# Optimization experiments

Hardware: AMD Instinct MI355X
Metric: run time of the kernel (lower is better)

Reference implementation:

```python
import jax, jax.numpy as jnp
import numpy as np

HEADS = 8

def setup_inputs() -> dict:
    key = jax.random.key(0)
    ks = jax.random.split(key, 4)
    N, C, H, W = 8, 256, 128, 128
    s = 0.02  # conv weight init scale
    return {
        "x":  jax.random.normal(ks[0], (N, C, H, W), dtype=jnp.float32),
        "Wk": jax.random.normal(ks[1], (C, C), dtype=jnp.float32) * s,
        "bk": jnp.zeros((C,), dtype=jnp.float32),
        "Wq": jax.random.normal(ks[2], (C, C), dtype=jnp.float32) * s,
        "bq": jnp.zeros((C,), dtype=jnp.float32),
        "Wv": jax.random.normal(ks[3], (C, C), dtype=jnp.float32) * s,
        "bv": jnp.zeros((C,), dtype=jnp.float32),
    }

def _conv1x1(x, Wt, b):
    # 1x1 conv == per-pixel GEMM: [N,C,H,W] x [D,C] -> [N,D,H,W]
    return jnp.einsum('nchw,dc->ndhw', x, Wt) + b[None, :, None, None]

def reference(x, Wk, bk, Wq, bq, Wv, bv):
    N, C, H, W = x.shape
    hc = C // HEADS          # head_channels
    L = H * W                # spatial tokens
    k = _conv1x1(x, Wk, bk).reshape(N, HEADS, hc, L)
    q = _conv1x1(x, Wq, bq).reshape(N, HEADS, hc, L)
    v = _conv1x1(x, Wv, bv).reshape(N, HEADS, hc, L)
    k = jax.nn.softmax(k, axis=3)   # softmax over spatial dim (keys)
    q = jax.nn.softmax(q, axis=2)   # softmax over channel dim within head (queries)
    # context = key @ value^T : [N,HEADS,hc_k,hc_v]
    ctx = jnp.einsum('nhkl,nhvl->nhkv', k, v)
    # attended = context^T @ query : [N,HEADS,hc_v,L]
    att = jnp.einsum('nhkv,nhkl->nhvl', ctx, q)
    att = att.reshape(N, C, H, W)
    # dim == out_channels -> reprojection is None; residual add
    return att + x
```

## Files before the change

kernel.cpp:

```cpp
#include <hip/hip_runtime.h>


typedef __attribute__((ext_vector_type(8))) short short8;
typedef __attribute__((ext_vector_type(4))) float f32x4;
typedef long long ll;

#define NB     8
#define CCH    256
#define LSP    16384
#define NHEADS 8
#define HC     32
#define NT     32
#define WSC    0.015625f

__device__ __forceinline__ unsigned short f2bf(float f) {
  union { float f; unsigned u; } v; v.f = f;
  unsigned r = v.u + 0x7fffu + ((v.u >> 16) & 1u);
  return (unsigned short)(r >> 16);
}
__device__ __forceinline__ unsigned cvt_pk_bf16(float lo, float hi) {
  unsigned r;
  asm("v_cvt_pk_bf16_f32 %0, %1, %2" : "=v"(r) : "v"(lo), "v"(hi));
  return r;
}
__device__ __forceinline__ unsigned char f2fp8(float f) {
  union { float f; unsigned u; } v; v.f = f;
  unsigned s = (v.u >> 24) & 0x80u;
  unsigned x = v.u & 0x7FFFFFFFu;
  if (x < 0x3C800000u) {
    float a = fabsf(f);
    int q = (int)rintf(a * 512.f);
    return (unsigned char)(s | (unsigned)q);
  }
  unsigned r = x + 0xFFFFFu + ((x >> 20) & 1u);
  unsigned e = r >> 23;
  unsigned m = (r >> 20) & 7u;
  int fe = (int)e - 120;
  if (fe > 15 || (fe == 15 && m == 7)) return (unsigned char)(s | 0x7Eu);
  return (unsigned char)(s | ((unsigned)fe << 3) | m);
}
__device__ __forceinline__ void gload_lds16(const unsigned char* g, unsigned char* l) {
  __builtin_amdgcn_global_load_lds(
      (const __attribute__((address_space(1))) unsigned int*)g,
      (__attribute__((address_space(3))) unsigned int*)l, 16, 0, 0);
}

__global__ void k_prep(const float* __restrict__ Wk, const float* __restrict__ bk,
                       const float* __restrict__ Wq, const float* __restrict__ bq,
                       const float* __restrict__ Wv, const float* __restrict__ bv,
                       unsigned char* __restrict__ Wb, float* __restrict__ bb,
                       float* __restrict__ ctx, float* __restrict__ S) {
  int idx = blockIdx.x * 256 + threadIdx.x;
  if (idx < NHEADS * 96 * CCH) {
    int c = idx & (CCH - 1);
    int row = (idx >> 8) % 96;
    int h = idx / (96 * CCH);
    int ch = h * HC;
    float val;
    if (row < HC)          val = Wk[(ch + row) * CCH + c];
    else if (row < 2 * HC) val = Wv[(ch + row - HC) * CCH + c];
    else                   val = Wq[(ch + row - 2 * HC) * CCH + c];
    Wb[idx] = f2fp8(val * 64.f);
  }
  if (idx < NHEADS * 96) {
    int row = idx % 96, h = idx / 96, ch = h * HC;
    float val;
    if (row < HC)          val = bk[ch + row];
    else if (row < 2 * HC) val = bv[ch + row - HC];
    else                   val = bq[ch + row - 2 * HC];
    bb[idx] = val;
  }
  if (idx < NB * NHEADS * HC * HC) ctx[idx] = 0.f;
  if (idx < NB * NHEADS * HC)      S[idx]   = 0.f;
}

__global__ __launch_bounds__(256)
void k_transpose(const float* __restrict__ x, unsigned char* __restrict__ xT) {
  __shared__ float tile[64][65];
  int b = blockIdx.x;
  int ct = b & 3;
  int lt = (b >> 2) & 255;
  int n  = b >> 10;
  int c0 = ct * 64, l0 = lt * 64;
  int t = threadIdx.x;
  int li = t & 63, cr = t >> 6;
  const float* xp = x + (size_t)n * CCH * LSP;
#pragma unroll
  for (int i = 0; i < 16; ++i) {
    int ci = cr * 16 + i;
    tile[ci][li] = xp[(size_t)(c0 + ci) * LSP + l0 + li];
  }
  __syncthreads();
  int cq = t & 15, lg = t >> 4;
  unsigned char* xo = xT + ((size_t)n * LSP + l0) * CCH + c0;
#pragma unroll
  for (int i = 0; i < 4; ++i) {
    int l = lg * 4 + i;
    unsigned pk = 0;
#pragma unroll
    for (int j = 0; j < 4; ++j)
      pk |= ((unsigned)f2fp8(tile[cq * 4 + j][l])) << (8 * j);
    *(unsigned*)&xo[(size_t)l * CCH + cq * 4] = pk;
  }
}

__global__ __launch_bounds__(512)
void k_fused(const unsigned char* __restrict__ xT,
             const unsigned char* __restrict__ Wb, const float* __restrict__ bb,
             unsigned short* __restrict__ qbuf, float* __restrict__ ctx,
             float* __restrict__ S) {
  __shared__ unsigned char wlds[96 * 256];
  __shared__ unsigned char xt[2][128 * 256];
  __shared__ unsigned short ekst[2][32][136];
  __shared__ unsigned short vst[2][32][136];

  int bid = (int)blockIdx.x;
  int h = bid >> 5;
  int r5 = bid & 31;
  int n = r5 >> 2, q2 = r5 & 3;
  int l0 = q2 << 12;
  int nh = n * NHEADS + h;
  int tid = threadIdx.x;
  int wid = tid >> 6, lane = tid & 63;
  int r16 = lane & 15, kg = lane >> 4;
  int rh = wid >> 2;
  int pq = wid & 3;

  const unsigned char* xTn = xT + ((size_t)n << 14) * CCH;
  const unsigned char* Wh = Wb + (size_t)h * 96 * CCH;

  auto stage_xt = [&](int buf, int tt) {
    int lb = l0 + tt * 128;
#pragma unroll
    for (int i = 0; i < 4; ++i) {
      int p = wid * 4 + i;
      int px = p * 4 + (lane >> 4);
      int c16 = lane & 15;
      gload_lds16(xTn + ((size_t)(lb + px) << 8) + ((c16 ^ (px & 7)) << 4),
                  &xt[buf][p * 1024]);
    }
  };

#pragma unroll
  for (int i = 0; i < 3; ++i) {
    int p = wid * 3 + i;
    int row = p * 4 + (lane >> 4);
    int c16 = lane & 15;
    gload_lds16(Wh + ((size_t)row << 8) + ((c16 ^ (row & 7)) << 4), &wlds[p * 1024]);
  }
  stage_xt(0, 0);
  stage_xt(1, 1);

  float bw[3];
#pragma unroll
  for (int m = 0; m < 3; ++m) bw[m] = bb[h * 96 + rh * 48 + m * 16 + r16];
  float bq[2][4];
#pragma unroll
  for (int m = 0; m < 2; ++m)
#pragma unroll
    for (int r = 0; r < 4; ++r) bq[m][r] = bb[h * 96 + 64 + m * 16 + kg * 4 + r];

  f32x4 actx = {0.f, 0.f, 0.f, 0.f};
  float sk0 = 0.f, sk1 = 0.f;

  asm volatile("s_waitcnt vmcnt(4)" ::: "memory");
  __builtin_amdgcn_sched_barrier(0);
  __builtin_amdgcn_s_barrier();
  __builtin_amdgcn_sched_barrier(0);

  const int base_w = (rh * 48 + r16) * 256;
  const int base_x = (pq * 32 + r16) * 256;
  int kh = pq >> 1, cvf = pq & 1;

  for (int t = 0; t < NT; ++t) {
    int cur = t & 1, sb = t & 1, pb = sb ^ 1;
    if (t) {
#pragma unroll
      for (int ks = 0; ks < 2; ++ks) {
        int col = kh * 64 + ks * 32 + kg * 8;
        short8 a = *(const short8*)&ekst[pb][rh * 16 + r16][col];
        short8 b = *(const short8*)&vst[pb][cvf * 16 + r16][col];
        actx = __builtin_amdgcn_mfma_f32_16x16x32_bf16(a, b, actx, 0, 0, 0);
      }
    }
    f32x4 acc[3][2];
#pragma unroll
    for (int m = 0; m < 3; ++m) { acc[m][0] = (f32x4){0,0,0,0}; acc[m][1] = (f32x4){0,0,0,0}; }
    const unsigned char* xb = &xt[cur][0];
#pragma unroll
    for (int kk = 0; kk < 8; ++kk) {
      int sw = (((kk * 2 + (kg >> 1)) ^ (r16 & 7)) << 4) + ((kg & 1) << 3);
      ll wf0 = *(const ll*)&wlds[base_w + sw];
      ll wf1 = *(const ll*)&wlds[base_w + 4096 + sw];
      ll wf2 = *(const ll*)&wlds[base_w + 8192 + sw];
      ll xf0 = *(const ll*)&xb[base_x + sw];
      ll xf1 = *(const ll*)&xb[base_x + 4096 + sw];
      if (rh == 0) {
        acc[0][0] = __builtin_amdgcn_mfma_f32_16x16x32_fp8_fp8(xf0, wf0, acc[0][0], 0, 0, 0);
        acc[0][1] = __builtin_amdgcn_mfma_f32_16x16x32_fp8_fp8(xf1, wf0, acc[0][1], 0, 0, 0);
        acc[1][0] = __builtin_amdgcn_mfma_f32_16x16x32_fp8_fp8(xf0, wf1, acc[1][0], 0, 0, 0);
        acc[1][1] = __builtin_amdgcn_mfma_f32_16x16x32_fp8_fp8(xf1, wf1, acc[1][1], 0, 0, 0);
        acc[2][0] = __builtin_amdgcn_mfma_f32_16x16x32_fp8_fp8(xf0, wf2, acc[2][0], 0, 0, 0);
        acc[2][1] = __builtin_amdgcn_mfma_f32_16x16x32_fp8_fp8(xf1, wf2, acc[2][1], 0, 0, 0);
      } else {
        acc[0][0] = __builtin_amdgcn_mfma_f32_16x16x32_fp8_fp8(xf0, wf0, acc[0][0], 0, 0, 0);
        acc[0][1] = __builtin_amdgcn_mfma_f32_16x16x32_fp8_fp8(xf1, wf0, acc[0][1], 0, 0, 0);
        acc[1][0] = __builtin_amdgcn_mfma_f32_16x16x32_fp8_fp8(wf1, xf0, acc[1][0], 0, 0, 0);
        acc[1][1] = __builtin_amdgcn_mfma_f32_16x16x32_fp8_fp8(wf1, xf1, acc[1][1], 0, 0, 0);
        acc[2][0] = __builtin_amdgcn_mfma_f32_16x16x32_fp8_fp8(wf2, xf0, acc[2][0], 0, 0, 0);
        acc[2][1] = __builtin_amdgcn_mfma_f32_16x16x32_fp8_fp8(wf2, xf1, acc[2][1], 0, 0, 0);
      }
    }
    __builtin_amdgcn_s_barrier();
    if (t + 2 < NT) stage_xt(cur, t + 2);

    if (rh == 0) {
#pragma unroll
      for (int nf = 0; nf < 2; ++nf) {
        int col = pq * 32 + nf * 16 + kg * 4;
#pragma unroll
        for (int m = 0; m < 2; ++m) {
          float e0 = __expf(acc[m][nf][0] * WSC + bw[m]);
          float e1 = __expf(acc[m][nf][1] * WSC + bw[m]);
          float e2 = __expf(acc[m][nf][2] * WSC + bw[m]);
          float e3 = __expf(acc[m][nf][3] * WSC + bw[m]);
          if (m == 0) sk0 += e0 + e1 + e2 + e3; else sk1 += e0 + e1 + e2 + e3;
          uint2 u = {cvt_pk_bf16(e0, e1), cvt_pk_bf16(e2, e3)};
          *(uint2*)&ekst[sb][m * 16 + r16][col] = u;
        }
        {
          float v0 = acc[2][nf][0] * WSC + bw[2], v1 = acc[2][nf][1] * WSC + bw[2];
          float v2 = acc[2][nf][2] * WSC + bw[2], v3 = acc[2][nf][3] * WSC + bw[2];
          uint2 u = {cvt_pk_bf16(v0, v1), cvt_pk_bf16(v2, v3)};
          *(uint2*)&vst[sb][r16][col] = u;
        }
      }
    } else {
#pragma unroll
      for (int nf = 0; nf < 2; ++nf) {
        int col = pq * 32 + nf * 16 + kg * 4;
        {
          float v0 = acc[0][nf][0] * WSC + bw[0], v1 = acc[0][nf][1] * WSC + bw[0];
          float v2 = acc[0][nf][2] * WSC + bw[0], v3 = acc[0][nf][3] * WSC + bw[0];
          uint2 u = {cvt_pk_bf16(v0, v1), cvt_pk_bf16(v2, v3)};
          *(uint2*)&vst[sb][16 + r16][col] = u;
        }
        float ea[4], eb[4];
        float s = 0.f;
#pragma unroll
        for (int r = 0; r < 4; ++r) {
          ea[r] = __expf(acc[1][nf][r] * WSC + bq[0][r]);
          eb[r] = __expf(acc[2][nf][r] * WSC + bq[1][r]);
          s += ea[r] + eb[r];
        }
        s += __shfl_xor(s, 16);
        s += __shfl_xor(s, 32);
        float inv = 1.f / s;
        int l = l0 + t * 128 + pq * 32 + nf * 16 + r16;
        unsigned short* qb = qbuf + (((size_t)nh * LSP + l) << 5);
        uint2 u0 = {cvt_pk_bf16(ea[0] * inv, ea[1] * inv), cvt_pk_bf16(ea[2] * inv, ea[3] * inv)};
        uint2 u1 = {cvt_pk_bf16(eb[0] * inv, eb[1] * inv), cvt_pk_bf16(eb[2] * inv, eb[3] * inv)};
        *(uint2*)&qb[kg * 4]      = u0;
        *(uint2*)&qb[16 + kg * 4] = u1;
      }
    }
    asm volatile("s_waitcnt lgkmcnt(0)" ::: "memory");
    __builtin_amdgcn_sched_barrier(0);
    if (t < NT - 2) {
      if (rh == 0) { asm volatile("s_waitcnt vmcnt(4)" ::: "memory"); }
      else         { asm volatile("s_waitcnt vmcnt(12)" ::: "memory"); }
    } else if (t == NT - 2) {
      if (rh == 0) { asm volatile("s_waitcnt vmcnt(0)" ::: "memory"); }
      else         { asm volatile("s_waitcnt vmcnt(8)" ::: "memory"); }
    }
    __builtin_amdgcn_sched_barrier(0);
    __builtin_amdgcn_s_barrier();
    __builtin_amdgcn_sched_barrier(0);
  }

#pragma unroll
  for (int ks = 0; ks < 2; ++ks) {
    int col = kh * 64 + ks * 32 + kg * 8;
    short8 a = *(const short8*)&ekst[(NT - 1) & 1][rh * 16 + r16][col];
    short8 b = *(const short8*)&vst[(NT - 1) & 1][cvf * 16 + r16][col];
    actx = __builtin_amdgcn_mfma_f32_16x16x32_bf16(a, b, actx, 0, 0, 0);
  }
  float* cp = ctx + ((size_t)nh << 10);
#pragma unroll
  for (int r = 0; r < 4; ++r)
    atomicAdd(&cp[(rh * 16 + kg * 4 + r) * HC + cvf * 16 + r16], actx[r]);
  if (rh == 0) {
    float s0 = sk0, s1 = sk1;
    s0 += __shfl_xor(s0, 16); s0 += __shfl_xor(s0, 32);
    s1 += __shfl_xor(s1, 16); s1 += __shfl_xor(s1, 32);
    if (kg == 0) {
      atomicAdd(&S[nh * HC + r16], s0);
      atomicAdd(&S[nh * HC + 16 + r16], s1);
    }
  }
}

__global__ void k_norm(const float* __restrict__ ctx, const float* __restrict__ S,
                       unsigned short* __restrict__ ctxT) {
  int idx = blockIdx.x * 256 + threadIdx.x;
  int cv = idx & 31, ck = (idx >> 5) & 31, nh = idx >> 10;
  float v = ctx[idx] / S[(nh << 5) + ck];
  ctxT[(nh << 10) + (cv << 5) + ck] = f2bf(v);
}

__global__ __launch_bounds__(256)
void k_att(const float* __restrict__ x, const unsigned short* __restrict__ qbuf,
           const unsigned short* __restrict__ ctxT, float* __restrict__ out) {
  int b = blockIdx.x;
  int lc = b & 63;
  int nh = b >> 6;
  int h = nh & 7, n = nh >> 3;
  int tid = threadIdx.x, wid = tid >> 6, lane = tid & 63;
  int r16 = lane & 15, kg = lane >> 4;
  int lw = lc * 256 + wid * 64;

  const unsigned short* cp = ctxT + ((size_t)nh << 10);
  short8 a0 = *(const short8*)&cp[(r16 << 5) + kg * 8];
  short8 a1 = *(const short8*)&cp[((16 + r16) << 5) + kg * 8];
  const unsigned short* qb = qbuf + (((size_t)nh * LSP) << 5);
  const float* xp = x   + ((size_t)n * CCH + (size_t)h * HC) * LSP;
  float*       op = out + ((size_t)n * CCH + (size_t)h * HC) * LSP;

#pragma unroll
  for (int t = 0; t < 4; ++t) {
    int l = lw + t * 16;
    short8 bf = *(const short8*)&qb[((size_t)(l + r16) << 5) + kg * 8];
    f32x4 d0 = {0, 0, 0, 0}, d1 = {0, 0, 0, 0};
    d0 = __builtin_amdgcn_mfma_f32_16x16x32_bf16(a0, bf, d0, 0, 0, 0);
    d1 = __builtin_amdgcn_mfma_f32_16x16x32_bf16(a1, bf, d1, 0, 0, 0);
#pragma unroll
    for (int r = 0; r < 4; ++r) {
      int cv = kg * 4 + r;
      int li = l + r16;
      op[(size_t)cv * LSP + li]        = d0[r] + xp[(size_t)cv * LSP + li];
      op[(size_t)(cv + 16) * LSP + li] = d1[r] + xp[(size_t)(cv + 16) * LSP + li];
    }
  }
}

extern "C" void kernel_launch(void* const* d_in, const int* in_sizes, int n_in,
                              void* d_out, int out_size, void* d_ws, size_t ws_size,
                              hipStream_t stream) {
  (void)in_sizes; (void)n_in; (void)out_size; (void)ws_size;
  const float* x  = (const float*)d_in[0];
  const float* Wk = (const float*)d_in[1];
  const float* bk = (const float*)d_in[2];
  const float* Wq = (const float*)d_in[3];
  const float* bq = (const float*)d_in[4];
  const float* Wv = (const float*)d_in[5];
  const float* bv = (const float*)d_in[6];
  float* out = (float*)d_out;

  char* ws = (char*)d_ws;
  unsigned char*  Wb   = (unsigned char*)(ws + 0);
  float*          bbp  = (float*)(ws + 196608);
  float*          ctx  = (float*)(ws + 199680);
  unsigned short* ctxT = (unsigned short*)(ws + 461824);
  float*          S    = (float*)(ws + 592896);
  unsigned short* qbuf = (unsigned short*)(ws + 601088);
  unsigned char*  xT   = (unsigned char*)(ws + 67709952);

  k_prep<<<768, 256, 0, stream>>>(Wk, bk, Wq, bq, Wv, bv, Wb, bbp, ctx, S);
  k_transpose<<<NB * 256 * 4, 256, 0, stream>>>(x, xT);
  k_fused<<<256, 512, 0, stream>>>(xT, Wb, bbp, qbuf, ctx, S);
  k_norm<<<256, 256, 0, stream>>>(ctx, S, ctxT);
  k_att<<<NB * NHEADS * 64, 256, 0, stream>>>(x, qbuf, ctxT, out);
}
```

Baseline: 193.9 us.

## Store queries and context in fp8, use hardware fp8 converts, rework LDS swizzles

The softmaxed query buffer and normalized context are now stored as fp8 instead of bf16, so the attention kernel runs fp8 MFMAs and reads half as many bytes of q. The transpose and q paths use the v_cvt_pk_fp8_f32 hardware instruction in place of software rounding. The LDS layouts for the e^k and v strips switch to a padded XOR swizzle, the x and W tile swizzles widen from 8 to 16 chunks, setprio is raised around the MFMA loop, and the vmcnt waits are changed to match the smaller store count. In exchange, fp8 for q and ctx loses precision, and hardware saturation and rounding may differ from the old software conversion.

```diff
diff --git a/kernel.cpp b/kernel.cpp
--- a/kernel.cpp
+++ b/kernel.cpp
@@ -21,6 +21,13 @@
 __device__ __forceinline__ unsigned cvt_pk_bf16(float lo, float hi) {
   unsigned r;
   asm("v_cvt_pk_bf16_f32 %0, %1, %2" : "=v"(r) : "v"(lo), "v"(hi));
+  return r;
+}
+__device__ __forceinline__ unsigned cvt4_fp8(float a, float b, float c, float d) {
+  unsigned r;
+  asm("v_cvt_pk_fp8_f32 %0, %1, %2\n\t"
+      "v_cvt_pk_fp8_f32 %0, %3, %4 op_sel:[0,0,1]"
+      : "=v"(r) : "v"(a), "v"(b), "v"(c), "v"(d));
   return r;
 }
 __device__ __forceinline__ unsigned char f2fp8(float f) {
@@ -43,6 +50,11 @@
   __builtin_amdgcn_global_load_lds(
       (const __attribute__((address_space(1))) unsigned int*)g,
       (__attribute__((address_space(3))) unsigned int*)l, 16, 0, 0);
+}
+__device__ __forceinline__ int strip_off(int row, int colsh) {
+  int byte = colsh * 2;
+  int chunk = byte >> 4;
+  return row * 272 + (((chunk ^ (row & 7)) << 4) | (byte & 15));
 }
 
 __global__ void k_prep(const float* __restrict__ Wk, const float* __restrict__ bk,
@@ -96,10 +108,8 @@
 #pragma unroll
   for (int i = 0; i < 4; ++i) {
     int l = lg * 4 + i;
-    unsigned pk = 0;
-#pragma unroll
-    for (int j = 0; j < 4; ++j)
-      pk |= ((unsigned)f2fp8(tile[cq * 4 + j][l])) << (8 * j);
+    unsigned pk = cvt4_fp8(tile[cq * 4][l], tile[cq * 4 + 1][l],
+                           tile[cq * 4 + 2][l], tile[cq * 4 + 3][l]);
     *(unsigned*)&xo[(size_t)l * CCH + cq * 4] = pk;
   }
 }
@@ -107,12 +117,12 @@
 __global__ __launch_bounds__(512)
 void k_fused(const unsigned char* __restrict__ xT,
              const unsigned char* __restrict__ Wb, const float* __restrict__ bb,
-             unsigned short* __restrict__ qbuf, float* __restrict__ ctx,
+             unsigned char* __restrict__ qbuf, float* __restrict__ ctx,
              float* __restrict__ S) {
   __shared__ unsigned char wlds[96 * 256];
   __shared__ unsigned char xt[2][128 * 256];
-  __shared__ unsigned short ekst[2][32][136];
-  __shared__ unsigned short vst[2][32][136];
+  __shared__ __align__(16) unsigned char ekst[2][32 * 272];
+  __shared__ __align__(16) unsigned char vst[2][32 * 272];
 
   int bid = (int)blockIdx.x;
   int h = bid >> 5;
@@ -136,7 +146,7 @@
       int p = wid * 4 + i;
       int px = p * 4 + (lane >> 4);
       int c16 = lane & 15;
-      gload_lds16(xTn + ((size_t)(lb + px) << 8) + ((c16 ^ (px & 7)) << 4),
+      gload_lds16(xTn + ((size_t)(lb + px) << 8) + ((c16 ^ (px & 15)) << 4),
                   &xt[buf][p * 1024]);
     }
   };
@@ -146,7 +156,7 @@
     int p = wid * 3 + i;
     int row = p * 4 + (lane >> 4);
     int c16 = lane & 15;
-    gload_lds16(Wh + ((size_t)row << 8) + ((c16 ^ (row & 7)) << 4), &wlds[p * 1024]);
+    gload_lds16(Wh + ((size_t)row << 8) + ((c16 ^ (row & 15)) << 4), &wlds[p * 1024]);
   }
   stage_xt(0, 0);
   stage_xt(1, 1);
@@ -177,9 +187,9 @@
     if (t) {
 #pragma unroll
       for (int ks = 0; ks < 2; ++ks) {
-        int col = kh * 64 + ks * 32 + kg * 8;
-        short8 a = *(const short8*)&ekst[pb][rh * 16 + r16][col];
-        short8 b = *(const short8*)&vst[pb][cvf * 16 + r16][col];
+        int colsh = kh * 64 + ks * 32 + kg * 8;
+        short8 a = *(const short8*)&ekst[pb][strip_off(rh * 16 + r16, colsh)];
+        short8 b = *(const short8*)&vst[pb][strip_off(cvf * 16 + r16, colsh)];
         actx = __builtin_amdgcn_mfma_f32_16x16x32_bf16(a, b, actx, 0, 0, 0);
       }
     }
@@ -187,9 +197,10 @@
 #pragma unroll
     for (int m = 0; m < 3; ++m) { acc[m][0] = (f32x4){0,0,0,0}; acc[m][1] = (f32x4){0,0,0,0}; }
     const unsigned char* xb = &xt[cur][0];
+    __builtin_amdgcn_s_setprio(1);
 #pragma unroll
     for (int kk = 0; kk < 8; ++kk) {
-      int sw = (((kk * 2 + (kg >> 1)) ^ (r16 & 7)) << 4) + ((kg & 1) << 3);
+      int sw = (((kk * 2 + (kg >> 1)) ^ r16) << 4) + ((kg & 1) << 3);
       ll wf0 = *(const ll*)&wlds[base_w + sw];
       ll wf1 = *(const ll*)&wlds[base_w + 4096 + sw];
       ll wf2 = *(const ll*)&wlds[base_w + 8192 + sw];
@@ -211,6 +222,7 @@
         acc[2][1] = __builtin_amdgcn_mfma_f32_16x16x32_fp8_fp8(wf2, xf1, acc[2][1], 0, 0, 0);
       }
     }
+    __builtin_amdgcn_s_setprio(0);
     __builtin_amdgcn_s_barrier();
     if (t + 2 < NT) stage_xt(cur, t + 2);
 
@@ -226,13 +238,13 @@
           float e3 = __expf(acc[m][nf][3] * WSC + bw[m]);
           if (m == 0) sk0 += e0 + e1 + e2 + e3; else sk1 += e0 + e1 + e2 + e3;
           uint2 u = {cvt_pk_bf16(e0, e1), cvt_pk_bf16(e2, e3)};
-          *(uint2*)&ekst[sb][m * 16 + r16][col] = u;
+          *(uint2*)&ekst[sb][strip_off(m * 16 + r16, col)] = u;
         }
         {
           float v0 = acc[2][nf][0] * WSC + bw[2], v1 = acc[2][nf][1] * WSC + bw[2];
           float v2 = acc[2][nf][2] * WSC + bw[2], v3 = acc[2][nf][3] * WSC + bw[2];
           uint2 u = {cvt_pk_bf16(v0, v1), cvt_pk_bf16(v2, v3)};
-          *(uint2*)&vst[sb][r16][col] = u;
+          *(uint2*)&vst[sb][strip_off(r16, col)] = u;
         }
       }
     } else {
@@ -243,7 +255,7 @@
           float v0 = acc[0][nf][0] * WSC + bw[0], v1 = acc[0][nf][1] * WSC + bw[0];
           float v2 = acc[0][nf][2] * WSC + bw[0], v3 = acc[0][nf][3] * WSC + bw[0];
           uint2 u = {cvt_pk_bf16(v0, v1), cvt_pk_bf16(v2, v3)};
-          *(uint2*)&vst[sb][16 + r16][col] = u;
+          *(uint2*)&vst[sb][strip_off(16 + r16, col)] = u;
         }
         float ea[4], eb[4];
         float s = 0.f;
@@ -257,21 +269,21 @@
         s += __shfl_xor(s, 32);
         float inv = 1.f / s;
         int l = l0 + t * 128 + pq * 32 + nf * 16 + r16;
-        unsigned short* qb = qbuf + (((size_t)nh * LSP + l) << 5);
-        uint2 u0 = {cvt_pk_bf16(ea[0] * inv, ea[1] * inv), cvt_pk_bf16(ea[2] * inv, ea[3] * inv)};
-        uint2 u1 = {cvt_pk_bf16(eb[0] * inv, eb[1] * inv), cvt_pk_bf16(eb[2] * inv, eb[3] * inv)};
-        *(uint2*)&qb[kg * 4]      = u0;
-        *(uint2*)&qb[16 + kg * 4] = u1;
+        unsigned char* qb = qbuf + (((size_t)nh * LSP + l) << 5);
+        unsigned u0 = cvt4_fp8(ea[0] * inv, ea[1] * inv, ea[2] * inv, ea[3] * inv);
+        unsigned u1 = cvt4_fp8(eb[0] * inv, eb[1] * inv, eb[2] * inv, eb[3] * inv);
+        *(unsigned*)&qb[kg * 4]      = u0;
+        *(unsigned*)&qb[16 + kg * 4] = u1;
       }
     }
     asm volatile("s_waitcnt lgkmcnt(0)" ::: "memory");
     __builtin_amdgcn_sched_barrier(0);
     if (t < NT - 2) {
       if (rh == 0) { asm volatile("s_waitcnt vmcnt(4)" ::: "memory"); }
-      else         { asm volatile("s_waitcnt vmcnt(12)" ::: "memory"); }
+      else         { asm volatile("s_waitcnt vmcnt(8)" ::: "memory"); }
     } else if (t == NT - 2) {
       if (rh == 0) { asm volatile("s_waitcnt vmcnt(0)" ::: "memory"); }
-      else         { asm volatile("s_waitcnt vmcnt(8)" ::: "memory"); }
+      else         { asm volatile("s_waitcnt vmcnt(4)" ::: "memory"); }
     }
     __builtin_amdgcn_sched_barrier(0);
     __builtin_amdgcn_s_barrier();
@@ -280,9 +292,9 @@
 
 #pragma unroll
   for (int ks = 0; ks < 2; ++ks) {
-    int col = kh * 64 + ks * 32 + kg * 8;
-    short8 a = *(const short8*)&ekst[(NT - 1) & 1][rh * 16 + r16][col];
-    short8 b = *(const short8*)&vst[(NT - 1) & 1][cvf * 16 + r16][col];
+    int colsh = kh * 64 + ks * 32 + kg * 8;
+    short8 a = *(const short8*)&ekst[(NT - 1) & 1][strip_off(rh * 16 + r16, colsh)];
+    short8 b = *(const short8*)&vst[(NT - 1) & 1][strip_off(cvf * 16 + r16, colsh)];
     actx = __builtin_amdgcn_mfma_f32_16x16x32_bf16(a, b, actx, 0, 0, 0);
   }
   float* cp = ctx + ((size_t)nh << 10);
@@ -301,16 +313,16 @@
 }
 
 __global__ void k_norm(const float* __restrict__ ctx, const float* __restrict__ S,
-                       unsigned short* __restrict__ ctxT) {
+                       unsigned char* __restrict__ ctxT) {
   int idx = blockIdx.x * 256 + threadIdx.x;
   int cv = idx & 31, ck = (idx >> 5) & 31, nh = idx >> 10;
   float v = ctx[idx] / S[(nh << 5) + ck];
-  ctxT[(nh << 10) + (cv << 5) + ck] = f2bf(v);
+  ctxT[(nh << 10) + (cv << 5) + ck] = f2fp8(v);
 }
 
 __global__ __launch_bounds__(256)
-void k_att(const float* __restrict__ x, const unsigned short* __restrict__ qbuf,
-           const unsigned short* __restrict__ ctxT, float* __restrict__ out) {
+void k_att(const float* __restrict__ x, const unsigned char* __restrict__ qbuf,
+           const unsigned char* __restrict__ ctxT, float* __restrict__ out) {
   int b = blockIdx.x;
   int lc = b & 63;
   int nh = b >> 6;
@@ -319,20 +331,20 @@
   int r16 = lane & 15, kg = lane >> 4;
   int lw = lc * 256 + wid * 64;
 
-  const unsigned short* cp = ctxT + ((size_t)nh << 10);
-  short8 a0 = *(const short8*)&cp[(r16 << 5) + kg * 8];
-  short8 a1 = *(const short8*)&cp[((16 + r16) << 5) + kg * 8];
-  const unsigned short* qb = qbuf + (((size_t)nh * LSP) << 5);
+  const unsigned char* cp = ctxT + ((size_t)nh << 10);
+  ll a0 = *(const ll*)&cp[(r16 << 5) + kg * 8];
+  ll a1 = *(const ll*)&cp[((16 + r16) << 5) + kg * 8];
+  const unsigned char* qb = qbuf + (((size_t)nh * LSP) << 5);
   const float* xp = x   + ((size_t)n * CCH + (size_t)h * HC) * LSP;
   float*       op = out + ((size_t)n * CCH + (size_t)h * HC) * LSP;
 
 #pragma unroll
   for (int t = 0; t < 4; ++t) {
     int l = lw + t * 16;
-    short8 bf = *(const short8*)&qb[((size_t)(l + r16) << 5) + kg * 8];
+    ll bq = *(const ll*)&qb[((size_t)(l + r16) << 5) + kg * 8];
     f32x4 d0 = {0, 0, 0, 0}, d1 = {0, 0, 0, 0};
-    d0 = __builtin_amdgcn_mfma_f32_16x16x32_bf16(a0, bf, d0, 0, 0, 0);
-    d1 = __builtin_amdgcn_mfma_f32_16x16x32_bf16(a1, bf, d1, 0, 0, 0);
+    d0 = __builtin_amdgcn_mfma_f32_16x16x32_fp8_fp8(a0, bq, d0, 0, 0, 0);
+    d1 = __builtin_amdgcn_mfma_f32_16x16x32_fp8_fp8(a1, bq, d1, 0, 0, 0);
 #pragma unroll
     for (int r = 0; r < 4; ++r) {
       int cv = kg * 4 + r;
@@ -360,10 +372,10 @@
   unsigned char*  Wb   = (unsigned char*)(ws + 0);
   float*          bbp  = (float*)(ws + 196608);
   float*          ctx  = (float*)(ws + 199680);
-  unsigned short* ctxT = (unsigned short*)(ws + 461824);
-  float*          S    = (float*)(ws + 592896);
-  unsigned short* qbuf = (unsigned short*)(ws + 601088);
-  unsigned char*  xT   = (unsigned char*)(ws + 67709952);
+  unsigned char*  ctxT = (unsigned char*)(ws + 461824);
+  float*          S    = (float*)(ws + 494592);
+  unsigned char*  qbuf = (unsigned char*)(ws + 502784);
+  unsigned char*  xT   = (unsigned char*)(ws + 34057216);
 
   k_prep<<<768, 256, 0, stream>>>(Wk, bk, Wq, bq, Wv, bv, Wb, bbp, ctx, S);
   k_transpose<<<NB * 256 * 4, 256, 0, stream>>>(x, xT);
```

Result: faster. 188.2 us (-2.9%).
